# Performance work log

Hardware: AMD Instinct MI355X
Metric: run time of the kernel (lower is better)

## Reference

```python
import jax, jax.numpy as jnp
import numpy as np

B, T, C = 512, 256, 384  # batch, seq (<= block_size 256), n_embed
HEAD = 64


def setup_inputs() -> dict:
    key = jax.random.key(0)
    k1, k2, k3, k4 = jax.random.split(key, 4)
    scale = 1.0 / np.sqrt(C)
    return {
        "x": jax.random.normal(k1, (B, T, C), dtype=jnp.float32),
        "Wq": jax.random.normal(k2, (C, HEAD), dtype=jnp.float32) * scale,
        "Wk": jax.random.normal(k3, (C, HEAD), dtype=jnp.float32) * scale,
        "Wv": jax.random.normal(k4, (C, HEAD), dtype=jnp.float32) * scale,
    }


def reference(x, Wq, Wk, Wv):
    # Single causal self-attention head (dropout in eval mode / identity).
    _, T_, C_ = x.shape
    q = x @ Wq  # [B,T,H]
    k = x @ Wk  # [B,T,H]
    v = x @ Wv  # [B,T,H]
    # NOTE: original scales by n_embed**-0.5 (C), not head_size**-0.5.
    wei = jnp.einsum('bth,bsh->bts', q, k) * (C_ ** -0.5)  # [B,T,T]
    causal = jnp.tril(jnp.ones((T_, T_), dtype=bool))
    wei = jnp.where(causal, wei, -jnp.inf)
    wei = jax.nn.softmax(wei, axis=-1)
    return jnp.einsum('bts,bsh->bth', wei, v)  # [B,T,H]
```

## Files before the change

kernel.cpp:

```cpp
#include <hip/hip_runtime.h>

#define B_ 512
#define T_ 256
#define C_ 384
#define H_ 64

typedef __attribute__((ext_vector_type(8))) short bf16x8;
typedef __attribute__((ext_vector_type(4))) float f32x4;

__device__ __forceinline__ short f2bf(float f) {
    unsigned u = __float_as_uint(f);
    u += 0x7fffu + ((u >> 16) & 1u);
    return (short)(u >> 16);
}

__device__ __forceinline__ unsigned long long pack4(float4 a) {
    return  (unsigned long long)(unsigned short)f2bf(a.x)
         | ((unsigned long long)(unsigned short)f2bf(a.y) << 16)
         | ((unsigned long long)(unsigned short)f2bf(a.z) << 32)
         | ((unsigned long long)(unsigned short)f2bf(a.w) << 48);
}

__global__ void pack_w_kernel(const float* __restrict__ Wq, const float* __restrict__ Wk,
                              const float* __restrict__ Wv, short* __restrict__ wp) {
    int p = blockIdx.x * 256 + threadIdx.x;
    if (p >= 12 * 12 * 512) return;
    int j    = p & 7;
    int lane = (p >> 3) & 63;
    int pc   = p >> 9;
    int ct = pc % 12, ks = pc / 12;
    int n  = ct * 16 + (lane & 15);
    int kk = ks * 32 + (lane >> 4) * 8 + j;
    const float* src = (n < 64) ? Wq : ((n < 128) ? Wk : Wv);
    wp[p] = f2bf(src[kk * 64 + (n & 63)]);
}

__global__ __launch_bounds__(1024, 4) void fused_kernel(
    const float* __restrict__ x, const short* __restrict__ wp,
    float* __restrict__ out) {
    __shared__ char lds_raw[118784];
    short* Qs = (short*)lds_raw;
    short* Ks = (short*)(lds_raw + 32768);
    short* Vs = (short*)(lds_raw + 65536);
    short* Pb = (short*)(lds_raw + 98304);

    const int b = blockIdx.x;
    const int tid = threadIdx.x;
    const int w = tid >> 6, lane = tid & 63;
    const int cl = lane & 15, quad = lane >> 4;

    const float* xb = x + (long)b * (T_ * C_);
    const float4* xb4 = (const float4*)xb;

    const int srow = w * 16 + quad;
    const unsigned st_even = (unsigned)(w * 2048 + quad * 128)
                           + (((unsigned)(cl >> 1) ^ (unsigned)quad) << 4)
                           + (unsigned)(lane & 1) * 8;
    const unsigned st_odd = st_even ^ 64u;

    const int rtb = (w & 3) * 4;
    const int ctb = (w >> 2) * 3;
    const unsigned abase = (unsigned)((rtb * 16 + cl) * 128)
                         + (((unsigned)quad ^ (unsigned)(cl & 7)) << 4);

    const short* wlB = wp + ctb * 512 + lane * 8;

    f32x4 acc[4][3];
    #pragma unroll
    for (int i = 0; i < 4; i++)
        #pragma unroll
        for (int j = 0; j < 3; j++) {
            f32x4 z = {0.f, 0.f, 0.f, 0.f};
            acc[i][j] = z;
        }

    {
        float4 sv[4];
        #pragma unroll
        for (int i = 0; i < 4; i++)
            sv[i] = xb4[(srow + i * 4) * 96 + cl];
        #pragma unroll
        for (int i = 0; i < 4; i++) {
            unsigned a = ((i & 1) ? st_odd : st_even) + (unsigned)i * 512u;
            *(unsigned long long*)(lds_raw + a) = pack4(sv[i]);
        }
    }
    __syncthreads();

    for (int c = 0; c < 6; ++c) {
        bf16x8 bfr[2][3];
        #pragma unroll
        for (int kl = 0; kl < 2; kl++) {
            const short* wk = wlB + (c * 2 + kl) * 6144;
            #pragma unroll
            for (int j = 0; j < 3; j++)
                bfr[kl][j] = *(const bf16x8*)(wk + j * 512);
        }

        float4 sv[4];
        if (c < 5) {
            #pragma unroll
            for (int i = 0; i < 4; i++)
                sv[i] = xb4[(srow + i * 4) * 96 + (c + 1) * 16 + cl];
        }

        const char* buf = lds_raw + (c & 1) * 32768;
        #pragma unroll
        for (int kl = 0; kl < 2; kl++) {
            bf16x8 af[4];
            #pragma unroll
            for (int i = 0; i < 4; i++)
                af[i] = *(const bf16x8*)(buf +
                    ((abase + (unsigned)i * 2048u) ^ (kl ? 64u : 0u)));
            #pragma unroll
            for (int i = 0; i < 4; i++)
                #pragma unroll
                for (int j = 0; j < 3; j++)
                    acc[i][j] = __builtin_amdgcn_mfma_f32_16x16x32_bf16(
                        af[i], bfr[kl][j], acc[i][j], 0, 0, 0);
        }

        if (c < 5) {
            char* nbuf = lds_raw + ((c + 1) & 1) * 32768;
            #pragma unroll
            for (int i = 0; i < 4; i++) {
                unsigned a = ((i & 1) ? st_odd : st_even) + (unsigned)i * 512u;
                *(unsigned long long*)(nbuf + a) = pack4(sv[i]);
            }
        }
        __syncthreads();
    }

    #pragma unroll
    for (int j = 0; j < 3; j++) {
        const int ct = ctb + j;
        if (ct < 4) {
            const int h = ct * 16 + cl;
            const int kk = h >> 5, hq = (h >> 3) & 3, jj = h & 7;
            #pragma unroll
            for (int i = 0; i < 4; i++)
                #pragma unroll
                for (int r = 0; r < 4; r++)
                    Qs[((rtb + i) * 2 + kk) * 512 + ((quad * 4 + r) + 16 * hq) * 8 + jj] =
                        f2bf(acc[i][j][r]);
        } else if (ct < 8) {
            const int h = (ct - 4) * 16 + cl;
            const int kk = h >> 5, hq = (h >> 3) & 3, jj = h & 7;
            #pragma unroll
            for (int i = 0; i < 4; i++)
                #pragma unroll
                for (int r = 0; r < 4; r++)
                    Ks[((rtb + i) * 2 + kk) * 512 + ((quad * 4 + r) + 16 * hq) * 8 + jj] =
                        f2bf(acc[i][j][r]);
        } else {
            const int ht = ct - 8;
            #pragma unroll
            for (int i = 0; i < 4; i++)
                #pragma unroll
                for (int r = 0; r < 4; r++) {
                    const int t = (rtb + i) * 16 + quad * 4 + r;
                    Vs[((t >> 5) * 4 + ht) * 512 + (cl + 16 * ((t >> 3) & 3)) * 8 + (t & 7)] =
                        f2bf(acc[i][j][r]);
                }
        }
    }

    __syncthreads();

    const float scale2 = 0.05103103630798287f * 1.4426950408889634f;

    const int rg = (w & 12) | ((w & 3) ^ (w >> 2));
    const int base = rg << 4;
    short* pb = Pb + w * 640;

    const bf16x8 qf0 = *(const bf16x8*)(Qs + (rg * 2 + 0) * 512 + lane * 8);
    const bf16x8 qf1 = *(const bf16x8*)(Qs + (rg * 2 + 1) * 512 + lane * 8);

    f32x4 sacc[16];
    #pragma unroll
    for (int st = 0; st < 16; st++) {
        if (st > rg) continue;
        bf16x8 k0 = *(const bf16x8*)(Ks + (st * 2 + 0) * 512 + lane * 8);
        bf16x8 k1 = *(const bf16x8*)(Ks + (st * 2 + 1) * 512 + lane * 8);
        f32x4 z = {0.f, 0.f, 0.f, 0.f};
        f32x4 t = __builtin_amdgcn_mfma_f32_16x16x32_bf16(qf0, k0, z, 0, 0, 0);
        t = __builtin_amdgcn_mfma_f32_16x16x32_bf16(qf1, k1, t, 0, 0, 0);
        sacc[st] = t;
    }

    float m4[4] = {-3e38f, -3e38f, -3e38f, -3e38f};
    #pragma unroll
    for (int st = 0; st < 16; st++) {
        if (st > rg) continue;
        #pragma unroll
        for (int r = 0; r < 4; r++) {
            float sv = sacc[st][r] * scale2;
            if (st * 16 + cl > base + quad * 4 + r) sv = -1e30f;
            sacc[st][r] = sv;
            m4[r] = fmaxf(m4[r], sv);
        }
    }
    #pragma unroll
    for (int d = 1; d < 16; d <<= 1)
        #pragma unroll
        for (int r = 0; r < 4; r++)
            m4[r] = fmaxf(m4[r], __shfl_xor(m4[r], d));

    float l4[4] = {0.f, 0.f, 0.f, 0.f};
    #pragma unroll
    for (int st = 0; st < 16; st++) {
        if (st > rg) continue;
        #pragma unroll
        for (int r = 0; r < 4; r++) {
            float pv = exp2f(sacc[st][r] - m4[r]);
            sacc[st][r] = pv;
            l4[r] += pv;
        }
    }
    #pragma unroll
    for (int d = 1; d < 16; d <<= 1)
        #pragma unroll
        for (int r = 0; r < 4; r++)
            l4[r] += __shfl_xor(l4[r], d);

    f32x4 oacc[4];
    #pragma unroll
    for (int ht = 0; ht < 4; ht++) {
        f32x4 z = {0.f, 0.f, 0.f, 0.f};
        oacc[ht] = z;
    }
    #pragma unroll
    for (int cc = 0; cc < 8; cc++) {
        if (cc > (rg >> 1)) continue;
        #pragma unroll
        for (int half = 0; half < 2; half++) {
            const int st = cc * 2 + half;
            #pragma unroll
            for (int r = 0; r < 4; r++) {
                short pv = (st <= rg) ? f2bf(sacc[st][r]) : (short)0;
                pb[(quad * 4 + r) * 40 + half * 16 + cl] = pv;
            }
        }
        __builtin_amdgcn_wave_barrier();
        const bf16x8 pa = *(const bf16x8*)(pb + cl * 40 + quad * 8);
        #pragma unroll
        for (int ht = 0; ht < 4; ht++) {
            const bf16x8 vf = *(const bf16x8*)(Vs + (cc * 4 + ht) * 512 + lane * 8);
            oacc[ht] = __builtin_amdgcn_mfma_f32_16x16x32_bf16(pa, vf, oacc[ht], 0, 0, 0);
        }
        __builtin_amdgcn_wave_barrier();
    }

    #pragma unroll
    for (int r = 0; r < 4; r++) {
        const float inv = 1.0f / l4[r];
        float* op = out + (long)(b * T_ + base + quad * 4 + r) * H_ + cl;
        #pragma unroll
        for (int ht = 0; ht < 4; ht++)
            op[ht * 16] = oacc[ht][r] * inv;
    }
}

extern "C" void kernel_launch(void* const* d_in, const int* in_sizes, int n_in,
                              void* d_out, int out_size, void* d_ws, size_t ws_size,
                              hipStream_t stream) {
    const float* x  = (const float*)d_in[0];
    const float* Wq = (const float*)d_in[1];
    const float* Wk = (const float*)d_in[2];
    const float* Wv = (const float*)d_in[3];
    float* out = (float*)d_out;

    short* wp = (short*)d_ws;

    pack_w_kernel<<<288, 256, 0, stream>>>(Wq, Wk, Wv, wp);
    fused_kernel<<<B_, 1024, 0, stream>>>(x, wp, out);
}
```

Before: 312.0 us.

## Restructure QKV projection to stage full-width 64-row x tiles in LDS

The QKV projection loop changes from iterating over six K-chunks of all 256 rows to four passes over 64-row tiles with the full 384-wide reduction staged in LDS. Each wave now keeps a 1x3 accumulator instead of 4x3, which lowers register pressure. The price is that weight fragments are reloaded from global memory on every pass (four times instead of once). LDS use grows to 144KB, and the P buffer now aliases the x staging area.

```diff
diff --git a/kernel.cpp b/kernel.cpp
--- a/kernel.cpp
+++ b/kernel.cpp
@@ -38,11 +38,12 @@
 __global__ __launch_bounds__(1024, 4) void fused_kernel(
     const float* __restrict__ x, const short* __restrict__ wp,
     float* __restrict__ out) {
-    __shared__ char lds_raw[118784];
-    short* Qs = (short*)lds_raw;
-    short* Ks = (short*)(lds_raw + 32768);
-    short* Vs = (short*)(lds_raw + 65536);
-    short* Pb = (short*)(lds_raw + 98304);
+    __shared__ char lds_raw[147456];
+    char*  Xb = lds_raw;
+    short* Qs = (short*)(lds_raw + 49152);
+    short* Ks = (short*)(lds_raw + 81920);
+    short* Vs = (short*)(lds_raw + 114688);
+    short* Pb = (short*)lds_raw;
 
     const int b = blockIdx.x;
     const int tid = threadIdx.x;
@@ -50,122 +51,101 @@
     const int cl = lane & 15, quad = lane >> 4;
 
     const float* xb = x + (long)b * (T_ * C_);
-    const float4* xb4 = (const float4*)xb;
-
-    const int srow = w * 16 + quad;
-    const unsigned st_even = (unsigned)(w * 2048 + quad * 128)
-                           + (((unsigned)(cl >> 1) ^ (unsigned)quad) << 4)
-                           + (unsigned)(lane & 1) * 8;
-    const unsigned st_odd = st_even ^ 64u;
-
-    const int rtb = (w & 3) * 4;
+    const float4* xq = (const float4*)xb + w * 384 + lane;
+
+    unsigned dst[6];
+    #pragma unroll
+    for (int i = 0; i < 6; i++) {
+        unsigned f = (unsigned)(w * 384 + i * 64 + lane);
+        unsigned r = f / 96u, c4 = f % 96u;
+        unsigned g = c4 >> 1, sub = c4 & 1u;
+        unsigned sw = (g & ~7u) | ((g & 7u) ^ (r & 7u));
+        dst[i] = r * 768u + sw * 16u + sub * 8u;
+    }
+
+    const int rt  = w & 3;
     const int ctb = (w >> 2) * 3;
-    const unsigned abase = (unsigned)((rtb * 16 + cl) * 128)
+    const unsigned addrA = (unsigned)((rt * 16 + cl) * 768)
                          + (((unsigned)quad ^ (unsigned)(cl & 7)) << 4);
 
     const short* wlB = wp + ctb * 512 + lane * 8;
 
-    f32x4 acc[4][3];
-    #pragma unroll
-    for (int i = 0; i < 4; i++)
+    {
+        float4 sv[6];
+        #pragma unroll
+        for (int i = 0; i < 6; i++) sv[i] = xq[i * 64];
+        #pragma unroll
+        for (int i = 0; i < 6; i++)
+            *(unsigned long long*)(Xb + dst[i]) = pack4(sv[i]);
+    }
+    __syncthreads();
+
+    for (int p = 0; p < 4; ++p) {
+        f32x4 acc[3];
         #pragma unroll
         for (int j = 0; j < 3; j++) {
             f32x4 z = {0.f, 0.f, 0.f, 0.f};
-            acc[i][j] = z;
-        }
-
-    {
-        float4 sv[4];
-        #pragma unroll
-        for (int i = 0; i < 4; i++)
-            sv[i] = xb4[(srow + i * 4) * 96 + cl];
-        #pragma unroll
-        for (int i = 0; i < 4; i++) {
-            unsigned a = ((i & 1) ? st_odd : st_even) + (unsigned)i * 512u;
-            *(unsigned long long*)(lds_raw + a) = pack4(sv[i]);
-        }
-    }
-    __syncthreads();
-
-    for (int c = 0; c < 6; ++c) {
-        bf16x8 bfr[2][3];
-        #pragma unroll
-        for (int kl = 0; kl < 2; kl++) {
-            const short* wk = wlB + (c * 2 + kl) * 6144;
-            #pragma unroll
-            for (int j = 0; j < 3; j++)
-                bfr[kl][j] = *(const bf16x8*)(wk + j * 512);
-        }
-
-        float4 sv[4];
-        if (c < 5) {
-            #pragma unroll
-            for (int i = 0; i < 4; i++)
-                sv[i] = xb4[(srow + i * 4) * 96 + (c + 1) * 16 + cl];
-        }
-
-        const char* buf = lds_raw + (c & 1) * 32768;
-        #pragma unroll
-        for (int kl = 0; kl < 2; kl++) {
-            bf16x8 af[4];
-            #pragma unroll
-            for (int i = 0; i < 4; i++)
-                af[i] = *(const bf16x8*)(buf +
-                    ((abase + (unsigned)i * 2048u) ^ (kl ? 64u : 0u)));
-            #pragma unroll
-            for (int i = 0; i < 4; i++)
-                #pragma unroll
-                for (int j = 0; j < 3; j++)
-                    acc[i][j] = __builtin_amdgcn_mfma_f32_16x16x32_bf16(
-                        af[i], bfr[kl][j], acc[i][j], 0, 0, 0);
-        }
-
-        if (c < 5) {
-            char* nbuf = lds_raw + ((c + 1) & 1) * 32768;
-            #pragma unroll
-            for (int i = 0; i < 4; i++) {
-                unsigned a = ((i & 1) ? st_odd : st_even) + (unsigned)i * 512u;
-                *(unsigned long long*)(nbuf + a) = pack4(sv[i]);
+            acc[j] = z;
+        }
+
+        float4 sv[6];
+        if (p < 3) {
+            #pragma unroll
+            for (int i = 0; i < 6; i++)
+                sv[i] = xq[(p + 1) * 6144 + i * 64];
+        }
+
+        #pragma unroll
+        for (int ks = 0; ks < 12; ks++) {
+            const unsigned aoff = (addrA + (unsigned)((ks >> 1) * 128))
+                                ^ (unsigned)((ks & 1) * 64);
+            const bf16x8 af = *(const bf16x8*)(Xb + aoff);
+            const short* wk = wlB + ks * 6144;
+            #pragma unroll
+            for (int j = 0; j < 3; j++) {
+                const bf16x8 bf = *(const bf16x8*)(wk + j * 512);
+                acc[j] = __builtin_amdgcn_mfma_f32_16x16x32_bf16(af, bf, acc[j], 0, 0, 0);
             }
         }
-        __syncthreads();
-    }
-
-    #pragma unroll
-    for (int j = 0; j < 3; j++) {
-        const int ct = ctb + j;
-        if (ct < 4) {
-            const int h = ct * 16 + cl;
-            const int kk = h >> 5, hq = (h >> 3) & 3, jj = h & 7;
-            #pragma unroll
-            for (int i = 0; i < 4; i++)
+
+        const int ts = p * 4 + rt;
+        #pragma unroll
+        for (int j = 0; j < 3; j++) {
+            const int ct = ctb + j;
+            if (ct < 4) {
+                const int h = ct * 16 + cl;
+                const int kk = h >> 5, hq = (h >> 3) & 3, jj = h & 7;
                 #pragma unroll
                 for (int r = 0; r < 4; r++)
-                    Qs[((rtb + i) * 2 + kk) * 512 + ((quad * 4 + r) + 16 * hq) * 8 + jj] =
-                        f2bf(acc[i][j][r]);
-        } else if (ct < 8) {
-            const int h = (ct - 4) * 16 + cl;
-            const int kk = h >> 5, hq = (h >> 3) & 3, jj = h & 7;
-            #pragma unroll
-            for (int i = 0; i < 4; i++)
+                    Qs[(ts * 2 + kk) * 512 + ((quad * 4 + r) + 16 * hq) * 8 + jj] =
+                        f2bf(acc[j][r]);
+            } else if (ct < 8) {
+                const int h = (ct - 4) * 16 + cl;
+                const int kk = h >> 5, hq = (h >> 3) & 3, jj = h & 7;
                 #pragma unroll
                 for (int r = 0; r < 4; r++)
-                    Ks[((rtb + i) * 2 + kk) * 512 + ((quad * 4 + r) + 16 * hq) * 8 + jj] =
-                        f2bf(acc[i][j][r]);
-        } else {
-            const int ht = ct - 8;
-            #pragma unroll
-            for (int i = 0; i < 4; i++)
+                    Ks[(ts * 2 + kk) * 512 + ((quad * 4 + r) + 16 * hq) * 8 + jj] =
+                        f2bf(acc[j][r]);
+            } else {
+                const int ht = ct - 8;
                 #pragma unroll
                 for (int r = 0; r < 4; r++) {
-                    const int t = (rtb + i) * 16 + quad * 4 + r;
+                    const int t = ts * 16 + quad * 4 + r;
                     Vs[((t >> 5) * 4 + ht) * 512 + (cl + 16 * ((t >> 3) & 3)) * 8 + (t & 7)] =
-                        f2bf(acc[i][j][r]);
+                        f2bf(acc[j][r]);
                 }
-        }
-    }
-
-    __syncthreads();
+            }
+        }
+
+        __syncthreads();
+
+        if (p < 3) {
+            #pragma unroll
+            for (int i = 0; i < 6; i++)
+                *(unsigned long long*)(Xb + dst[i]) = pack4(sv[i]);
+            __syncthreads();
+        }
+    }
 
     const float scale2 = 0.05103103630798287f * 1.4426950408889634f;
 
```

Result: slower. 473.3 us (+51.7%).
